# Kernel optimization log

Hardware: AMD Instinct MI355X
Metric: run time of the kernel (lower is better)

The kernel has to match this reference:

```python
import math
import jax, jax.numpy as jnp
import numpy as np

B, T, C = 2, 2048, 4096
H = 32
D = C // H  # head_dim = 128


def compute_freq(dim, max_len, theta=10000):
    freq = 1.0 / theta ** (jnp.arange(0, dim, 2, dtype=jnp.float32) / dim)
    t = jnp.arange(max_len, dtype=jnp.float32)
    m = jnp.einsum('i,j->ij', t, freq)          # [L, dim/2]
    m = jnp.concatenate([m, m], axis=-1)         # [L, dim]
    return jnp.cos(m), jnp.sin(m)


def rotate_half(x):
    # Faithful to source: depth = full last dim, so x1 is the whole tensor
    # and x2 is empty -> rotate_half(x) == x (a quirk of the original code).
    depth = x.shape[-1]
    x1 = x[..., :depth]
    x2 = x[..., depth:]
    return jnp.concatenate([-x2, x1], axis=-1)


def setup_inputs() -> dict:
    key = jax.random.key(0)
    kx, kq, kk, kv, ko = jax.random.split(key, 5)
    std = 0.02
    input_ids = jax.random.normal(kx, (B, T, C), dtype=jnp.float32)
    Wq = jax.random.normal(kq, (C, C), dtype=jnp.float32) * std
    Wk = jax.random.normal(kk, (C, C), dtype=jnp.float32) * std
    Wv = jax.random.normal(kv, (C, C), dtype=jnp.float32) * std
    Wo = jax.random.normal(ko, (C, C), dtype=jnp.float32) * std
    # Additive causal mask, as typically passed to this module.
    causal = jnp.tril(jnp.ones((T, T), dtype=bool))
    attention_mask = jnp.where(causal, 0.0, -1e9).astype(jnp.float32)[None, None]
    return {"input_ids": input_ids, "Wq": Wq, "Wk": Wk, "Wv": Wv,
            "Wo": Wo, "attention_mask": attention_mask}


def reference(input_ids, Wq, Wk, Wv, Wo, attention_mask):
    b, t, c = input_ids.shape
    # QKV projections (no bias), reshape to [b, h, t, d]
    q = (input_ids @ Wq).reshape(b, t, H, D).swapaxes(1, 2)
    k = (input_ids @ Wk).reshape(b, t, H, D).swapaxes(1, 2)
    v = (input_ids @ Wv).reshape(b, t, H, D).swapaxes(1, 2)
    # Inline RoPE (faithful, including the source's rotate_half behavior)
    cos, sin = compute_freq(D, t)                # [t, D]
    q = q * cos + rotate_half(q) * sin
    k = k * cos + rotate_half(k) * sin
    # Naive full attention
    attn = jnp.einsum('bhqd,bhkd->bhqk', q, k) / math.sqrt(D)
    attn = attn + attention_mask
    attn = jax.nn.softmax(attn, axis=-1)
    out = jnp.einsum('bhqk,bhkd->bhqd', attn, v)
    out = out.swapaxes(1, 2).reshape(b, t, c)
    return out @ Wo
```

## Files before the change

### kernel.cpp

```cpp
#include <hip/hip_runtime.h>
#include <hip/hip_bf16.h>

#define B_ 2
#define T_ 2048
#define C_ 4096
#define H_ 32
#define D_ 128

typedef __bf16 bf16x8 __attribute__((ext_vector_type(8)));
typedef float f32x4 __attribute__((ext_vector_type(4)));

__device__ __forceinline__ void gload_lds16(const void* g, void* l) {
  __builtin_amdgcn_global_load_lds(
      (const __attribute__((address_space(1))) void*)g,
      (__attribute__((address_space(3))) void*)l, 16, 0, 0);
}

__device__ __forceinline__ ushort f2bf(float f) {
  union { float f; uint u; } x; x.f = f;
  uint r = x.u + 0x7FFFu + ((x.u >> 16) & 1u);
  return (ushort)(r >> 16);
}

__global__ __launch_bounds__(256) void cvt_f32_bf16(
    const float* __restrict__ in, ushort* __restrict__ out)
{
  long i = ((long)blockIdx.x * 256 + threadIdx.x) * 8;
  float4 a = *(const float4*)&in[i];
  float4 b = *(const float4*)&in[i + 4];
  union { ushort u[8]; uint4 v; } g;
  g.u[0] = f2bf(a.x); g.u[1] = f2bf(a.y); g.u[2] = f2bf(a.z); g.u[3] = f2bf(a.w);
  g.u[4] = f2bf(b.x); g.u[5] = f2bf(b.y); g.u[6] = f2bf(b.z); g.u[7] = f2bf(b.w);
  *(uint4*)&out[i] = g.v;
}

__global__ __launch_bounds__(256) void transpose_f32_bf16(
    const float* __restrict__ in, ushort* __restrict__ out, int ldi, int ldo)
{
  __shared__ __align__(16) ushort tile[64][72];
  const float* ip = in + (long)blockIdx.y * 64 * ldi + (long)blockIdx.x * 64;
  ushort* op = out + (long)blockIdx.x * 64 * ldo + (long)blockIdx.y * 64;
  const int t = threadIdx.x;
  const int row = t >> 2, c0 = (t & 3) * 16;
#pragma unroll
  for (int v = 0; v < 4; ++v) {
    float4 f = *(const float4*)&ip[(long)row * ldi + c0 + v * 4];
    ushort4 w;
    w.x = f2bf(f.x); w.y = f2bf(f.y); w.z = f2bf(f.z); w.w = f2bf(f.w);
    *(ushort4*)&tile[row][c0 + v * 4] = w;
  }
  __syncthreads();
#pragma unroll
  for (int i = 0; i < 2; ++i) {
    int t2 = i * 256 + t;
    int orow = t2 >> 3, ch = t2 & 7;
    union { ushort u[8]; uint4 v; } g;
#pragma unroll
    for (int e = 0; e < 8; ++e) g.u[e] = tile[ch * 8 + e][orow];
    *(uint4*)&op[(long)orow * ldo + ch * 8] = g.v;
  }
}

__global__ __launch_bounds__(256) void transpose_bf16(
    const ushort* __restrict__ in, ushort* __restrict__ out,
    int ldi, int ldo, long zi1, long zi2, long zo1, long zo2)
{
  __shared__ __align__(16) ushort tile[64][72];
  const int z = blockIdx.z;
  const long z1 = z & 31, z2 = z >> 5;
  const ushort* ip = in + z1 * zi1 + z2 * zi2 +
                     (long)blockIdx.y * 64 * ldi + (long)blockIdx.x * 64;
  ushort* op = out + z1 * zo1 + z2 * zo2 +
               (long)blockIdx.x * 64 * ldo + (long)blockIdx.y * 64;
  const int t = threadIdx.x;
#pragma unroll
  for (int i = 0; i < 2; ++i) {
    int t2 = i * 256 + t;
    int row = t2 >> 3, ch = t2 & 7;
    *(uint4*)&tile[row][ch * 8] = *(const uint4*)&ip[(long)row * ldi + ch * 8];
  }
  __syncthreads();
#pragma unroll
  for (int i = 0; i < 2; ++i) {
    int t2 = i * 256 + t;
    int orow = t2 >> 3, ch = t2 & 7;
    union { ushort u[8]; uint4 v; } g;
#pragma unroll
    for (int e = 0; e < 8; ++e) g.u[e] = tile[ch * 8 + e][orow];
    *(uint4*)&op[(long)orow * ldo + ch * 8] = g.v;
  }
}

#define STAGE_A(h, tt) do {                                                    \
    __hip_bfloat16* dst_ = AS + ((((tt) & 1) * 2 + (h)) * 8192) + w * 512;     \
    const __hip_bfloat16* src_ = Asrc + (size_t)((h) * 128) * K + (size_t)(tt) * 64; \
    gload_lds16(src_, dst_);                                                   \
    gload_lds16(src_ + (size_t)64 * K, dst_ + 4096);                           \
  } while (0)

#define STAGE_B(h, tt) do {                                                    \
    __hip_bfloat16* dst_ = BS + ((((tt) & 1) * 2 + (h)) * 8192) + w * 512;     \
    const __hip_bfloat16* src_ = Bsrc + (size_t)((h) * 128) * K + (size_t)(tt) * 64; \
    gload_lds16(src_, dst_);                                                   \
    gload_lds16(src_ + (size_t)64 * K, dst_ + 4096);                           \
  } while (0)

#define MFMA16(pM, pN, AF, BF)                                                 \
  _Pragma("unroll")                                                            \
  for (int mf = 0; mf < 4; ++mf)                                               \
    _Pragma("unroll")                                                          \
    for (int nf = 0; nf < 2; ++nf)                                             \
      _Pragma("unroll")                                                        \
      for (int ks = 0; ks < 2; ++ks)                                           \
        acc[pM][pN][mf][nf] = __builtin_amdgcn_mfma_f32_16x16x32_bf16(         \
            AF[mf][ks], BF[nf][ks], acc[pM][pN][mf][nf], 0, 0, 0);

template <typename OutT>
__global__ __launch_bounds__(512, 2) void gemm256(
    const __hip_bfloat16* __restrict__ A,
    const __hip_bfloat16* __restrict__ Bt,
    OutT* __restrict__ C,
    int M, int N, int K, int rope_mode)
{
  extern __shared__ __hip_bfloat16 smem[];
  __hip_bfloat16* AS = smem;
  __hip_bfloat16* BS = smem + 32768;

  const int tid = threadIdx.x, lane = tid & 63, w = tid >> 6;
  const int wm = w >> 2, wn = w & 3;
  const int fr = lane & 15, quad = lane >> 4;

  const int bid = blockIdx.x;
  const int s = (bid & 7) * 32 + (bid >> 3);
  const int m0 = (s >> 4) * 256, n0 = (s & 15) * 256;

  const int srow = tid >> 3;
  const int schunk = ((tid & 7) ^ (srow & 7)) * 8;
  const __hip_bfloat16* Asrc = A + (size_t)(m0 + srow) * K + schunk;
  const __hip_bfloat16* Bsrc = Bt + (size_t)(n0 + srow) * K + schunk;

  f32x4 acc[2][2][4][2] = {};

  STAGE_A(0, 0); STAGE_B(0, 0); STAGE_A(1, 0); STAGE_B(1, 0);
  STAGE_A(0, 1); STAGE_B(0, 1); STAGE_A(1, 1); STAGE_B(1, 1);
  asm volatile("s_waitcnt vmcnt(8)" ::: "memory");
  asm volatile("s_barrier" ::: "memory");

  const int NT = K >> 6;
  for (int t = 0; t < NT; ++t) {
    const __hip_bfloat16* As0 = AS + (t & 1) * 16384;
    const __hip_bfloat16* Bs0 = BS + (t & 1) * 16384;
    bf16x8 af[4][2], b0[2][2], b1[2][2];

#pragma unroll
    for (int mf = 0; mf < 4; ++mf) {
      const int row = wm * 64 + mf * 16 + fr;
#pragma unroll
      for (int ks = 0; ks < 2; ++ks)
        af[mf][ks] = *(const bf16x8*)
            &As0[row * 64 + (((ks * 4 + quad) ^ (fr & 7)) << 3)];
    }
#pragma unroll
    for (int nf = 0; nf < 2; ++nf) {
      const int row = wn * 32 + nf * 16 + fr;
#pragma unroll
      for (int ks = 0; ks < 2; ++ks)
        b0[nf][ks] = *(const bf16x8*)
            &Bs0[row * 64 + (((ks * 4 + quad) ^ (fr & 7)) << 3)];
    }
    asm volatile("s_barrier" ::: "memory");
    asm volatile("s_waitcnt lgkmcnt(0)" ::: "memory");
    __builtin_amdgcn_s_setprio(1);
    MFMA16(0, 0, af, b0)
    __builtin_amdgcn_s_setprio(0);
    asm volatile("s_barrier" ::: "memory");

#pragma unroll
    for (int nf = 0; nf < 2; ++nf) {
      const int row = wn * 32 + nf * 16 + fr;
#pragma unroll
      for (int ks = 0; ks < 2; ++ks)
        b1[nf][ks] = *(const bf16x8*)
            &Bs0[8192 + row * 64 + (((ks * 4 + quad) ^ (fr & 7)) << 3)];
    }
    if (t + 2 < NT) { STAGE_B(0, t + 2); STAGE_A(0, t + 2); }
    asm volatile("s_barrier" ::: "memory");
    asm volatile("s_waitcnt lgkmcnt(0)" ::: "memory");
    __builtin_amdgcn_s_setprio(1);
    MFMA16(0, 1, af, b1)
    __builtin_amdgcn_s_setprio(0);
    asm volatile("s_barrier" ::: "memory");

#pragma unroll
    for (int mf = 0; mf < 4; ++mf) {
      const int row = wm * 64 + mf * 16 + fr;
#pragma unroll
      for (int ks = 0; ks < 2; ++ks)
        af[mf][ks] = *(const bf16x8*)
            &As0[8192 + row * 64 + (((ks * 4 + quad) ^ (fr & 7)) << 3)];
    }
    if (t + 2 < NT) STAGE_B(1, t + 2);
    asm volatile("s_barrier" ::: "memory");
    asm volatile("s_waitcnt lgkmcnt(0)" ::: "memory");
    __builtin_amdgcn_s_setprio(1);
    MFMA16(1, 1, af, b1)
    __builtin_amdgcn_s_setprio(0);
    asm volatile("s_barrier" ::: "memory");

    if (t + 2 < NT) STAGE_A(1, t + 2);
    if (t < NT - 2) asm volatile("s_waitcnt vmcnt(8)" ::: "memory");
    else            asm volatile("s_waitcnt vmcnt(0)" ::: "memory");
    asm volatile("s_barrier" ::: "memory");
    __builtin_amdgcn_s_setprio(1);
    MFMA16(1, 0, af, b0)
    __builtin_amdgcn_s_setprio(0);
    asm volatile("s_barrier" ::: "memory");
  }

  const float gscale = (rope_mode == 1) ? 0.08838834764831845f : 1.0f;
  float freqv[2] = {0.f, 0.f};
  if (rope_mode) {
#pragma unroll
    for (int nf = 0; nf < 2; ++nf)
      freqv[nf] = exp2f((float)((wn & 1) * 32 + nf * 16 + fr) *
                        -0.20762050593046012f);
  }
#pragma unroll
  for (int pM = 0; pM < 2; ++pM)
#pragma unroll
    for (int mf = 0; mf < 4; ++mf)
#pragma unroll
      for (int r = 0; r < 4; ++r) {
        const int grow = m0 + pM * 128 + wm * 64 + mf * 16 + quad * 4 + r;
        float fct[2] = {1.f, 1.f};
        if (rope_mode) {
          const int tt = grow & (T_ - 1);
#pragma unroll
          for (int nf = 0; nf < 2; ++nf) {
            float sn, cs;
            sincosf((float)tt * freqv[nf], &sn, &cs);
            fct[nf] = (cs + sn) * gscale;
          }
        }
#pragma unroll
        for (int pN = 0; pN < 2; ++pN)
#pragma unroll
          for (int nf = 0; nf < 2; ++nf) {
            const int col = n0 + pN * 128 + wn * 32 + nf * 16 + fr;
            float v = acc[pM][pN][mf][nf][r] * fct[nf];
            if constexpr (sizeof(OutT) == 4)
              C[(size_t)grow * N + col] = v;
            else
              C[(size_t)grow * N + col] = __float2bfloat16(v);
          }
      }
}

__global__ __launch_bounds__(256, 2) void flash_attn(
    const __hip_bfloat16* __restrict__ Q,
    const __hip_bfloat16* __restrict__ K,
    const __hip_bfloat16* __restrict__ Vt,
    __hip_bfloat16* __restrict__ O)
{
  __shared__ __align__(16) __hip_bfloat16 Ks[128 * 128];
  __shared__ __align__(16) __hip_bfloat16 Ps[4][32 * 64];
  const int tid = threadIdx.x, lane = tid & 63, wid = tid >> 6;
  const int bx = blockIdx.x, bh = blockIdx.y;
  const int b = bh >> 5, h = bh & 31;
  const int fr = lane & 15;
  const int quad = lane >> 4;
  const __hip_bfloat16* Kbase = K + (size_t)(b * T_) * C_ + h * D_;
  const __hip_bfloat16* Vbase = Vt + (size_t)bh * D_ * T_;

  const int strow = wid * 32 + quad;

  for (int pass = 0; pass < 2; ++pass) {
    const int qt = pass ? (15 - bx) : bx;
    const int q0 = qt * 128;
    const __hip_bfloat16* Qbase = Q + (size_t)(b * T_ + q0) * C_ + h * D_;

#pragma unroll
    for (int j = 0; j < 8; ++j) {
      const int swz = quad + (j & 1) * 4;
      gload_lds16(Qbase + (size_t)(strow + j * 4) * C_ + ((fr ^ swz) * 8),
                  &Ks[(wid * 8 + j) * 512]);
    }
    __syncthreads();
    bf16x8 qf[2][4];
#pragma unroll
    for (int mi = 0; mi < 2; ++mi)
#pragma unroll
      for (int ks = 0; ks < 4; ++ks)
        qf[mi][ks] = *(const bf16x8*)&Ks[(wid * 32 + mi * 16 + fr) * 128 +
                                         (((ks * 4 + quad) ^ (fr & 7)) << 3)];
    __syncthreads();

    float m_i[2][4], l_i[2][4];
#pragma unroll
    for (int mi = 0; mi < 2; ++mi)
#pragma unroll
      for (int r = 0; r < 4; ++r) { m_i[mi][r] = -1e30f; l_i[mi][r] = 0.f; }
    f32x4 oa[2][8] = {};

    for (int kt = 0; kt <= qt; ++kt) {
#pragma unroll
      for (int j = 0; j < 8; ++j) {
        const int swz = quad + (j & 1) * 4;
        gload_lds16(
            Kbase + (size_t)(kt * 128 + strow + j * 4) * C_ + ((fr ^ swz) * 8),
            &Ks[(wid * 8 + j) * 512]);
      }
      __syncthreads();

      f32x4 s[2][8] = {};
#pragma unroll
      for (int ks = 0; ks < 4; ++ks) {
        bf16x8 kf[8];
#pragma unroll
        for (int ni = 0; ni < 8; ++ni)
          kf[ni] = *(const bf16x8*)&Ks[(ni * 16 + fr) * 128 +
                                       (((ks * 4 + quad) ^ (fr & 7)) << 3)];
        __builtin_amdgcn_s_setprio(1);
#pragma unroll
        for (int mi = 0; mi < 2; ++mi)
#pragma unroll
          for (int ni = 0; ni < 8; ++ni)
            s[mi][ni] = __builtin_amdgcn_mfma_f32_16x16x32_bf16(
                qf[mi][ks], kf[ni], s[mi][ni], 0, 0, 0);
        __builtin_amdgcn_s_setprio(0);
      }
      __syncthreads();

#pragma unroll
      for (int j = 0; j < 8; ++j) {
        const int swz = quad + (j & 1) * 4;
        gload_lds16(
            Vbase + (size_t)(strow + j * 4) * T_ + kt * 128 + ((fr ^ swz) * 8),
            &Ks[(wid * 8 + j) * 512]);
      }

      if (kt == qt) {
#pragma unroll
        for (int mi = 0; mi < 2; ++mi)
#pragma unroll
          for (int ni = 0; ni < 8; ++ni)
#pragma unroll
            for (int r = 0; r < 4; ++r) {
              int rl = wid * 32 + mi * 16 + quad * 4 + r;
              int cl = ni * 16 + fr;
              if (cl > rl) s[mi][ni][r] = -1e30f;
            }
      }

#pragma unroll
      for (int mi = 0; mi < 2; ++mi)
#pragma unroll
        for (int r = 0; r < 4; ++r) {
          float mx = -1e30f;
#pragma unroll
          for (int ni = 0; ni < 8; ++ni) mx = fmaxf(mx, s[mi][ni][r]);
          mx = fmaxf(mx, __shfl_xor(mx, 1, 16));
          mx = fmaxf(mx, __shfl_xor(mx, 2, 16));
          mx = fmaxf(mx, __shfl_xor(mx, 4, 16));
          mx = fmaxf(mx, __shfl_xor(mx, 8, 16));
          float mnew = fmaxf(m_i[mi][r], mx);
          float alpha = __expf(m_i[mi][r] - mnew);
          float rs = 0.f;
#pragma unroll
          for (int ni = 0; ni < 8; ++ni) {
            float p = __expf(s[mi][ni][r] - mnew);
            s[mi][ni][r] = p;
            rs += p;
          }
          rs += __shfl_xor(rs, 1, 16);
          rs += __shfl_xor(rs, 2, 16);
          rs += __shfl_xor(rs, 4, 16);
          rs += __shfl_xor(rs, 8, 16);
          m_i[mi][r] = mnew;
          l_i[mi][r] = l_i[mi][r] * alpha + rs;
#pragma unroll
          for (int ni = 0; ni < 8; ++ni) oa[mi][ni][r] *= alpha;
        }

#pragma unroll
      for (int hh = 0; hh < 2; ++hh) {
#pragma unroll
        for (int mi = 0; mi < 2; ++mi)
#pragma unroll
          for (int l = 0; l < 4; ++l) {
            const int sw = (l ^ quad) & 3;
#pragma unroll
            for (int r = 0; r < 4; ++r)
              Ps[wid][(mi * 16 + quad * 4 + r) * 64 + sw * 16 + fr] =
                  __float2bfloat16(s[mi][hh * 4 + l][r]);
          }
        if (hh == 0) __syncthreads();
#pragma unroll
        for (int kl = 0; kl < 2; ++kl) {
          const int ks = hh * 2 + kl;
          bf16x8 pf[2], vf[8];
#pragma unroll
          for (int mi = 0; mi < 2; ++mi) {
            const int rowl = mi * 16 + fr;
            const int sw = ((kl * 2 + (quad >> 1)) ^ ((fr >> 2) & 3)) & 3;
            pf[mi] = *(const bf16x8*)
                &Ps[wid][rowl * 64 + sw * 16 + (quad & 1) * 8];
          }
#pragma unroll
          for (int ni = 0; ni < 8; ++ni)
            vf[ni] = *(const bf16x8*)&Ks[(ni * 16 + fr) * 128 +
                                         (((ks * 4 + quad) ^ (fr & 7)) << 3)];
          __builtin_amdgcn_s_setprio(1);
#pragma unroll
          for (int mi = 0; mi < 2; ++mi)
#pragma unroll
            for (int ni = 0; ni < 8; ++ni)
              oa[mi][ni] = __builtin_amdgcn_mfma_f32_16x16x32_bf16(
                  pf[mi], vf[ni], oa[mi][ni], 0, 0, 0);
          __builtin_amdgcn_s_setprio(0);
        }
      }
      __syncthreads();
    }

#pragma unroll
    for (int mi = 0; mi < 2; ++mi)
#pragma unroll
      for (int r = 0; r < 4; ++r) {
        float inv = 1.f / l_i[mi][r];
        int grow = b * T_ + q0 + wid * 32 + mi * 16 + quad * 4 + r;
#pragma unroll
        for (int ni = 0; ni < 8; ++ni)
          O[(size_t)grow * C_ + h * D_ + ni * 16 + fr] =
              __float2bfloat16(oa[mi][ni][r] * inv);
      }
  }
}

extern "C" void kernel_launch(void* const* d_in, const int* in_sizes, int n_in,
                              void* d_out, int out_size, void* d_ws, size_t ws_size,
                              hipStream_t stream) {
  const float* X  = (const float*)d_in[0];
  const float* Wq = (const float*)d_in[1];
  const float* Wk = (const float*)d_in[2];
  const float* Wv = (const float*)d_in[3];
  const float* Wo = (const float*)d_in[4];
  float* out = (float*)d_out;

  char* ws = (char*)d_ws;
  const size_t SZ = (size_t)4096 * 4096 * 2;
  __hip_bfloat16* Xb  = (__hip_bfloat16*)(ws);
  __hip_bfloat16* Wt  = (__hip_bfloat16*)(ws + SZ);
  __hip_bfloat16* Qb  = (__hip_bfloat16*)(ws + 2 * SZ);
  __hip_bfloat16* Kb  = (__hip_bfloat16*)(ws + 3 * SZ);
  __hip_bfloat16* Vb  = (__hip_bfloat16*)(ws + 4 * SZ);
  __hip_bfloat16* Vtb = Xb;
  __hip_bfloat16* Ob  = Vb;

  const dim3 blk(256);
  const dim3 gT(64, 64, 1);

  hipFuncSetAttribute(reinterpret_cast<const void*>(&gemm256<__hip_bfloat16>),
                      hipFuncAttributeMaxDynamicSharedMemorySize, 131072);
  hipFuncSetAttribute(reinterpret_cast<const void*>(&gemm256<float>),
                      hipFuncAttributeMaxDynamicSharedMemorySize, 131072);

  cvt_f32_bf16<<<8192, blk, 0, stream>>>(X, (ushort*)Xb);

  transpose_f32_bf16<<<gT, blk, 0, stream>>>(Wq, (ushort*)Wt, 4096, 4096);
  gemm256<__hip_bfloat16><<<dim3(256), dim3(512), 131072, stream>>>(
      Xb, Wt, Qb, 4096, 4096, 4096, 1);
  transpose_f32_bf16<<<gT, blk, 0, stream>>>(Wk, (ushort*)Wt, 4096, 4096);
  gemm256<__hip_bfloat16><<<dim3(256), dim3(512), 131072, stream>>>(
      Xb, Wt, Kb, 4096, 4096, 4096, 2);
  transpose_f32_bf16<<<gT, blk, 0, stream>>>(Wv, (ushort*)Wt, 4096, 4096);
  gemm256<__hip_bfloat16><<<dim3(256), dim3(512), 131072, stream>>>(
      Xb, Wt, Vb, 4096, 4096, 4096, 0);

  transpose_bf16<<<dim3(2, 32, 64), blk, 0, stream>>>(
      (const ushort*)Vb, (ushort*)Vtb, 4096, 2048,
       128,  8388608,  262144,  8388608);

  flash_attn<<<dim3(8, 64), blk, 0, stream>>>(Qb, Kb, Vtb, Ob);

  transpose_f32_bf16<<<gT, blk, 0, stream>>>(Wo, (ushort*)Wt, 4096, 4096);
  gemm256<float><<<dim3(256), dim3(512), 131072, stream>>>(
      Ob, Wt, out, 4096, 4096, 4096, 0);
}
```

Measured before the change: 1.014 ms.

## Fuse Q/K/V projections into one 768-block GEMM with 32-wide K tiles

Result: slower. 1.093 ms (+7.7%).

```diff
diff --git a/kernel.cpp b/kernel.cpp
--- a/kernel.cpp
+++ b/kernel.cpp
@@ -91,14 +91,14 @@
   }
 }
 
-#define STAGE_A(h, tt) do {                                                    \
+#define STAGE_A64(h, tt) do {                                                  \
     __hip_bfloat16* dst_ = AS + ((((tt) & 1) * 2 + (h)) * 8192) + w * 512;     \
     const __hip_bfloat16* src_ = Asrc + (size_t)((h) * 128) * K + (size_t)(tt) * 64; \
     gload_lds16(src_, dst_);                                                   \
     gload_lds16(src_ + (size_t)64 * K, dst_ + 4096);                           \
   } while (0)
 
-#define STAGE_B(h, tt) do {                                                    \
+#define STAGE_B64(h, tt) do {                                                  \
     __hip_bfloat16* dst_ = BS + ((((tt) & 1) * 2 + (h)) * 8192) + w * 512;     \
     const __hip_bfloat16* src_ = Bsrc + (size_t)((h) * 128) * K + (size_t)(tt) * 64; \
     gload_lds16(src_, dst_);                                                   \
@@ -141,8 +141,8 @@
 
   f32x4 acc[2][2][4][2] = {};
 
-  STAGE_A(0, 0); STAGE_B(0, 0); STAGE_A(1, 0); STAGE_B(1, 0);
-  STAGE_A(0, 1); STAGE_B(0, 1); STAGE_A(1, 1); STAGE_B(1, 1);
+  STAGE_A64(0, 0); STAGE_B64(0, 0); STAGE_A64(1, 0); STAGE_B64(1, 0);
+  STAGE_A64(0, 1); STAGE_B64(0, 1); STAGE_A64(1, 1); STAGE_B64(1, 1);
   asm volatile("s_waitcnt vmcnt(8)" ::: "memory");
   asm volatile("s_barrier" ::: "memory");
 
@@ -183,7 +183,7 @@
         b1[nf][ks] = *(const bf16x8*)
             &Bs0[8192 + row * 64 + (((ks * 4 + quad) ^ (fr & 7)) << 3)];
     }
-    if (t + 2 < NT) { STAGE_B(0, t + 2); STAGE_A(0, t + 2); }
+    if (t + 2 < NT) { STAGE_B64(0, t + 2); STAGE_A64(0, t + 2); }
     asm volatile("s_barrier" ::: "memory");
     asm volatile("s_waitcnt lgkmcnt(0)" ::: "memory");
     __builtin_amdgcn_s_setprio(1);
@@ -199,7 +199,7 @@
         af[mf][ks] = *(const bf16x8*)
             &As0[8192 + row * 64 + (((ks * 4 + quad) ^ (fr & 7)) << 3)];
     }
-    if (t + 2 < NT) STAGE_B(1, t + 2);
+    if (t + 2 < NT) STAGE_B64(1, t + 2);
     asm volatile("s_barrier" ::: "memory");
     asm volatile("s_waitcnt lgkmcnt(0)" ::: "memory");
     __builtin_amdgcn_s_setprio(1);
@@ -207,7 +207,7 @@
     __builtin_amdgcn_s_setprio(0);
     asm volatile("s_barrier" ::: "memory");
 
-    if (t + 2 < NT) STAGE_A(1, t + 2);
+    if (t + 2 < NT) STAGE_A64(1, t + 2);
     if (t < NT - 2) asm volatile("s_waitcnt vmcnt(8)" ::: "memory");
     else            asm volatile("s_waitcnt vmcnt(0)" ::: "memory");
     asm volatile("s_barrier" ::: "memory");
@@ -252,6 +252,159 @@
               C[(size_t)grow * N + col] = v;
             else
               C[(size_t)grow * N + col] = __float2bfloat16(v);
+          }
+      }
+}
+
+#define STAGE_A32(h, tt) do {                                                  \
+    __hip_bfloat16* dst_ = AS + ((((tt) & 1) * 2 + (h)) * 4096) + w * 512;     \
+    gload_lds16(Asrc + (size_t)((h) * 128) * K + (size_t)(tt) * 32, dst_);     \
+  } while (0)
+
+#define STAGE_B32(h, tt) do {                                                  \
+    __hip_bfloat16* dst_ = BS + ((((tt) & 1) * 2 + (h)) * 4096) + w * 512;     \
+    gload_lds16(Bsrc + (size_t)((h) * 128) * K + (size_t)(tt) * 32, dst_);     \
+  } while (0)
+
+#define MFMA8(pM, pN, AF, BF)                                                  \
+  _Pragma("unroll")                                                            \
+  for (int mf = 0; mf < 4; ++mf)                                               \
+    _Pragma("unroll")                                                          \
+    for (int nf = 0; nf < 2; ++nf)                                             \
+      acc[pM][pN][mf][nf] = __builtin_amdgcn_mfma_f32_16x16x32_bf16(           \
+          AF[mf], BF[nf], acc[pM][pN][mf][nf], 0, 0, 0);
+
+__global__ __launch_bounds__(512, 2) void gemm256_qkv(
+    const __hip_bfloat16* __restrict__ A,
+    const __hip_bfloat16* __restrict__ Bq,
+    const __hip_bfloat16* __restrict__ Bk,
+    const __hip_bfloat16* __restrict__ Bv,
+    __hip_bfloat16* __restrict__ Cq,
+    __hip_bfloat16* __restrict__ Ck,
+    __hip_bfloat16* __restrict__ Cv,
+    int N, int K)
+{
+  extern __shared__ __hip_bfloat16 smem[];
+  __hip_bfloat16* AS = smem;
+  __hip_bfloat16* BS = smem + 16384;
+
+  const int tid = threadIdx.x, lane = tid & 63, w = tid >> 6;
+  const int wm = w >> 2, wn = w & 3;
+  const int fr = lane & 15, quad = lane >> 4;
+
+  const int bid = blockIdx.x;
+  const int s = (bid & 7) * 96 + (bid >> 3);
+  const int mi = s / 48, ni = s % 48;
+  const int m0 = mi * 256;
+  const int wsel = ni >> 4;
+  const int n0 = (ni & 15) * 256;
+  const __hip_bfloat16* Bt = wsel == 0 ? Bq : (wsel == 1 ? Bk : Bv);
+  __hip_bfloat16* C = wsel == 0 ? Cq : (wsel == 1 ? Ck : Cv);
+  const int rope_mode = wsel == 0 ? 1 : (wsel == 1 ? 2 : 0);
+
+  const int srow = tid >> 2;
+  const int schunk = ((tid & 3) ^ (srow & 3)) * 8;
+  const __hip_bfloat16* Asrc = A + (size_t)(m0 + srow) * K + schunk;
+  const __hip_bfloat16* Bsrc = Bt + (size_t)(n0 + srow) * K + schunk;
+
+  f32x4 acc[2][2][4][2] = {};
+
+  STAGE_A32(0, 0); STAGE_B32(0, 0); STAGE_A32(1, 0); STAGE_B32(1, 0);
+  STAGE_A32(0, 1); STAGE_B32(0, 1); STAGE_A32(1, 1); STAGE_B32(1, 1);
+  asm volatile("s_waitcnt vmcnt(4)" ::: "memory");
+  asm volatile("s_barrier" ::: "memory");
+
+  const int NT = K >> 5;
+  for (int t = 0; t < NT; ++t) {
+    const __hip_bfloat16* As0 = AS + (t & 1) * 8192;
+    const __hip_bfloat16* Bs0 = BS + (t & 1) * 8192;
+    bf16x8 af[4], b0[2], b1[2];
+
+#pragma unroll
+    for (int mf = 0; mf < 4; ++mf) {
+      const int row = wm * 64 + mf * 16 + fr;
+      af[mf] = *(const bf16x8*)&As0[row * 32 + ((quad ^ (fr & 3)) << 3)];
+    }
+#pragma unroll
+    for (int nf = 0; nf < 2; ++nf) {
+      const int row = wn * 32 + nf * 16 + fr;
+      b0[nf] = *(const bf16x8*)&Bs0[row * 32 + ((quad ^ (fr & 3)) << 3)];
+    }
+    asm volatile("s_barrier" ::: "memory");
+    asm volatile("s_waitcnt lgkmcnt(0)" ::: "memory");
+    __builtin_amdgcn_s_setprio(1);
+    MFMA8(0, 0, af, b0)
+    __builtin_amdgcn_s_setprio(0);
+    asm volatile("s_barrier" ::: "memory");
+
+#pragma unroll
+    for (int nf = 0; nf < 2; ++nf) {
+      const int row = wn * 32 + nf * 16 + fr;
+      b1[nf] = *(const bf16x8*)&Bs0[4096 + row * 32 + ((quad ^ (fr & 3)) << 3)];
+    }
+    if (t + 2 < NT) { STAGE_B32(0, t + 2); STAGE_A32(0, t + 2); }
+    asm volatile("s_barrier" ::: "memory");
+    asm volatile("s_waitcnt lgkmcnt(0)" ::: "memory");
+    __builtin_amdgcn_s_setprio(1);
+    MFMA8(0, 1, af, b1)
+    __builtin_amdgcn_s_setprio(0);
+    asm volatile("s_barrier" ::: "memory");
+
+#pragma unroll
+    for (int mf = 0; mf < 4; ++mf) {
+      const int row = wm * 64 + mf * 16 + fr;
+      af[mf] = *(const bf16x8*)&As0[4096 + row * 32 + ((quad ^ (fr & 3)) << 3)];
+    }
+    if (t + 2 < NT) STAGE_B32(1, t + 2);
+    asm volatile("s_barrier" ::: "memory");
+    asm volatile("s_waitcnt lgkmcnt(0)" ::: "memory");
+    __builtin_amdgcn_s_setprio(1);
+    MFMA8(1, 1, af, b1)
+    __builtin_amdgcn_s_setprio(0);
+    asm volatile("s_barrier" ::: "memory");
+
+    if (t + 2 < NT) STAGE_A32(1, t + 2);
+    if (t < NT - 2) asm volatile("s_waitcnt vmcnt(4)" ::: "memory");
+    else            asm volatile("s_waitcnt vmcnt(0)" ::: "memory");
+    asm volatile("s_barrier" ::: "memory");
+    __builtin_amdgcn_s_setprio(1);
+    MFMA8(1, 0, af, b0)
+    __builtin_amdgcn_s_setprio(0);
+    asm volatile("s_barrier" ::: "memory");
+  }
+
+  const float gscale = (rope_mode == 1) ? 0.08838834764831845f : 1.0f;
+  float freqv[2] = {0.f, 0.f};
+  if (rope_mode) {
+#pragma unroll
+    for (int nf = 0; nf < 2; ++nf)
+      freqv[nf] = exp2f((float)((wn & 1) * 32 + nf * 16 + fr) *
+                        -0.20762050593046012f);
+  }
+#pragma unroll
+  for (int pM = 0; pM < 2; ++pM)
+#pragma unroll
+    for (int mf = 0; mf < 4; ++mf)
+#pragma unroll
+      for (int r = 0; r < 4; ++r) {
+        const int grow = m0 + pM * 128 + wm * 64 + mf * 16 + quad * 4 + r;
+        float fct[2] = {1.f, 1.f};
+        if (rope_mode) {
+          const int tt = grow & (T_ - 1);
+#pragma unroll
+          for (int nf = 0; nf < 2; ++nf) {
+            float sn, cs;
+            sincosf((float)tt * freqv[nf], &sn, &cs);
+            fct[nf] = (cs + sn) * gscale;
+          }
+        }
+#pragma unroll
+        for (int pN = 0; pN < 2; ++pN)
+#pragma unroll
+          for (int nf = 0; nf < 2; ++nf) {
+            const int col = n0 + pN * 128 + wn * 32 + nf * 16 + fr;
+            C[(size_t)grow * N + col] =
+                __float2bfloat16(acc[pM][pN][mf][nf][r] * fct[nf]);
           }
       }
 }
@@ -449,14 +602,6 @@
 
   char* ws = (char*)d_ws;
   const size_t SZ = (size_t)4096 * 4096 * 2;
-  __hip_bfloat16* Xb  = (__hip_bfloat16*)(ws);
-  __hip_bfloat16* Wt  = (__hip_bfloat16*)(ws + SZ);
-  __hip_bfloat16* Qb  = (__hip_bfloat16*)(ws + 2 * SZ);
-  __hip_bfloat16* Kb  = (__hip_bfloat16*)(ws + 3 * SZ);
-  __hip_bfloat16* Vb  = (__hip_bfloat16*)(ws + 4 * SZ);
-  __hip_bfloat16* Vtb = Xb;
-  __hip_bfloat16* Ob  = Vb;
-
   const dim3 blk(256);
   const dim3 gT(64, 64, 1);
 
@@ -464,26 +609,63 @@
                       hipFuncAttributeMaxDynamicSharedMemorySize, 131072);
   hipFuncSetAttribute(reinterpret_cast<const void*>(&gemm256<float>),
                       hipFuncAttributeMaxDynamicSharedMemorySize, 131072);
-
-  cvt_f32_bf16<<<8192, blk, 0, stream>>>(X, (ushort*)Xb);
-
-  transpose_f32_bf16<<<gT, blk, 0, stream>>>(Wq, (ushort*)Wt, 4096, 4096);
-  gemm256<__hip_bfloat16><<<dim3(256), dim3(512), 131072, stream>>>(
-      Xb, Wt, Qb, 4096, 4096, 4096, 1);
-  transpose_f32_bf16<<<gT, blk, 0, stream>>>(Wk, (ushort*)Wt, 4096, 4096);
-  gemm256<__hip_bfloat16><<<dim3(256), dim3(512), 131072, stream>>>(
-      Xb, Wt, Kb, 4096, 4096, 4096, 2);
-  transpose_f32_bf16<<<gT, blk, 0, stream>>>(Wv, (ushort*)Wt, 4096, 4096);
-  gemm256<__hip_bfloat16><<<dim3(256), dim3(512), 131072, stream>>>(
-      Xb, Wt, Vb, 4096, 4096, 4096, 0);
-
-  transpose_bf16<<<dim3(2, 32, 64), blk, 0, stream>>>(
-      (const ushort*)Vb, (ushort*)Vtb, 4096, 2048,
-       128,  8388608,  262144,  8388608);
-
-  flash_attn<<<dim3(8, 64), blk, 0, stream>>>(Qb, Kb, Vtb, Ob);
-
-  transpose_f32_bf16<<<gT, blk, 0, stream>>>(Wo, (ushort*)Wt, 4096, 4096);
-  gemm256<float><<<dim3(256), dim3(512), 131072, stream>>>(
-      Ob, Wt, out, 4096, 4096, 4096, 0);
-}
+  hipFuncSetAttribute(reinterpret_cast<const void*>(&gemm256_qkv),
+                      hipFuncAttributeMaxDynamicSharedMemorySize, 65536);
+
+  if (ws_size >= 7 * SZ) {
+    __hip_bfloat16* Xb  = (__hip_bfloat16*)(ws);
+    __hip_bfloat16* Wqt = (__hip_bfloat16*)(ws + SZ);
+    __hip_bfloat16* Wkt = (__hip_bfloat16*)(ws + 2 * SZ);
+    __hip_bfloat16* Wvt = (__hip_bfloat16*)(ws + 3 * SZ);
+    __hip_bfloat16* Qb  = (__hip_bfloat16*)(ws + 4 * SZ);
+    __hip_bfloat16* Kb  = (__hip_bfloat16*)(ws + 5 * SZ);
+    __hip_bfloat16* Vb  = (__hip_bfloat16*)(ws + 6 * SZ);
+    __hip_bfloat16* Vtb = Xb;
+    __hip_bfloat16* Ob  = Vb;
+    __hip_bfloat16* Wt  = Wkt;
+
+    cvt_f32_bf16<<<8192, blk, 0, stream>>>(X, (ushort*)Xb);
+    transpose_f32_bf16<<<gT, blk, 0, stream>>>(Wq, (ushort*)Wqt, 4096, 4096);
+    transpose_f32_bf16<<<gT, blk, 0, stream>>>(Wk, (ushort*)Wkt, 4096, 4096);
+    transpose_f32_bf16<<<gT, blk, 0, stream>>>(Wv, (ushort*)Wvt, 4096, 4096);
+
+    gemm256_qkv<<<dim3(768), dim3(512), 65536, stream>>>(
+        Xb, Wqt, Wkt, Wvt, Qb, Kb, Vb, 4096, 4096);
+
+    transpose_bf16<<<dim3(2, 32, 64), blk, 0, stream>>>(
+        (const ushort*)Vb, (ushort*)Vtb, 4096, 2048,
+        128, 8388608, 262144, 8388608);
+
+    flash_attn<<<dim3(8, 64), blk, 0, stream>>>(Qb, Kb, Vtb, Ob);
+
+    transpose_f32_bf16<<<gT, blk, 0, stream>>>(Wo, (ushort*)Wt, 4096, 4096);
+    gemm256<float><<<dim3(256), dim3(512), 131072, stream>>>(
+        Ob, Wt, out, 4096, 4096, 4096, 0);
+  } else {
+    __hip_bfloat16* Xb  = (__hip_bfloat16*)(ws);
+    __hip_bfloat16* Wt  = (__hip_bfloat16*)(ws + SZ);
+    __hip_bfloat16* Qb  = (__hip_bfloat16*)(ws + 2 * SZ);
+    __hip_bfloat16* Kb  = (__hip_bfloat16*)(ws + 3 * SZ);
+    __hip_bfloat16* Vb  = (__hip_bfloat16*)(ws + 4 * SZ);
+    __hip_bfloat16* Vtb = Xb;
+    __hip_bfloat16* Ob  = Vb;
+
+    cvt_f32_bf16<<<8192, blk, 0, stream>>>(X, (ushort*)Xb);
+    transpose_f32_bf16<<<gT, blk, 0, stream>>>(Wq, (ushort*)Wt, 4096, 4096);
+    gemm256<__hip_bfloat16><<<dim3(256), dim3(512), 131072, stream>>>(
+        Xb, Wt, Qb, 4096, 4096, 4096, 1);
+    transpose_f32_bf16<<<gT, blk, 0, stream>>>(Wk, (ushort*)Wt, 4096, 4096);
+    gemm256<__hip_bfloat16><<<dim3(256), dim3(512), 131072, stream>>>(
+        Xb, Wt, Kb, 4096, 4096, 4096, 2);
+    transpose_f32_bf16<<<gT, blk, 0, stream>>>(Wv, (ushort*)Wt, 4096, 4096);
+    gemm256<__hip_bfloat16><<<dim3(256), dim3(512), 131072, stream>>>(
+        Xb, Wt, Vb, 4096, 4096, 4096, 0);
+    transpose_bf16<<<dim3(2, 32, 64), blk, 0, stream>>>(
+        (const ushort*)Vb, (ushort*)Vtb, 4096, 2048,
+        128, 8388608, 262144, 8388608);
+    flash_attn<<<dim3(8, 64), blk, 0, stream>>>(Qb, Kb, Vtb, Ob);
+    transpose_f32_bf16<<<gT, blk, 0, stream>>>(Wo, (ushort*)Wt, 4096, 4096);
+    gemm256<float><<<dim3(256), dim3(512), 131072, stream>>>(
+        Ob, Wt, out, 4096, 4096, 4096, 0);
+  }
+}
```

## Fuse Q, K, V projections into one 768-block GEMM launch

Applied to the files above, without the earlier changes.

Measured after the change: 1.024 ms. About the same (+1.0%).

```diff
diff --git a/kernel.cpp b/kernel.cpp
--- a/kernel.cpp
+++ b/kernel.cpp
@@ -91,14 +91,14 @@
   }
 }
 
-#define STAGE_A(h, tt) do {                                                    \
+#define STAGE_A64(h, tt) do {                                                  \
     __hip_bfloat16* dst_ = AS + ((((tt) & 1) * 2 + (h)) * 8192) + w * 512;     \
     const __hip_bfloat16* src_ = Asrc + (size_t)((h) * 128) * K + (size_t)(tt) * 64; \
     gload_lds16(src_, dst_);                                                   \
     gload_lds16(src_ + (size_t)64 * K, dst_ + 4096);                           \
   } while (0)
 
-#define STAGE_B(h, tt) do {                                                    \
+#define STAGE_B64(h, tt) do {                                                  \
     __hip_bfloat16* dst_ = BS + ((((tt) & 1) * 2 + (h)) * 8192) + w * 512;     \
     const __hip_bfloat16* src_ = Bsrc + (size_t)((h) * 128) * K + (size_t)(tt) * 64; \
     gload_lds16(src_, dst_);                                                   \
@@ -114,6 +114,118 @@
       for (int ks = 0; ks < 2; ++ks)                                           \
         acc[pM][pN][mf][nf] = __builtin_amdgcn_mfma_f32_16x16x32_bf16(         \
             AF[mf][ks], BF[nf][ks], acc[pM][pN][mf][nf], 0, 0, 0);
+
+#define GEMM_KLOOP()                                                           \
+  STAGE_A64(0, 0); STAGE_B64(0, 0); STAGE_A64(1, 0); STAGE_B64(1, 0);          \
+  STAGE_A64(0, 1); STAGE_B64(0, 1); STAGE_A64(1, 1); STAGE_B64(1, 1);          \
+  asm volatile("s_waitcnt vmcnt(8)" ::: "memory");                             \
+  asm volatile("s_barrier" ::: "memory");                                      \
+  const int NT = K >> 6;                                                       \
+  for (int t = 0; t < NT; ++t) {                                               \
+    const __hip_bfloat16* As0 = AS + (t & 1) * 16384;                          \
+    const __hip_bfloat16* Bs0 = BS + (t & 1) * 16384;                          \
+    bf16x8 af[4][2], b0[2][2], b1[2][2];                                       \
+    _Pragma("unroll")                                                          \
+    for (int mf = 0; mf < 4; ++mf) {                                           \
+      const int row = wm * 64 + mf * 16 + fr;                                  \
+      _Pragma("unroll")                                                        \
+      for (int ks = 0; ks < 2; ++ks)                                           \
+        af[mf][ks] = *(const bf16x8*)                                          \
+            &As0[row * 64 + (((ks * 4 + quad) ^ (fr & 7)) << 3)];              \
+    }                                                                          \
+    _Pragma("unroll")                                                          \
+    for (int nf = 0; nf < 2; ++nf) {                                           \
+      const int row = wn * 32 + nf * 16 + fr;                                  \
+      _Pragma("unroll")                                                        \
+      for (int ks = 0; ks < 2; ++ks)                                           \
+        b0[nf][ks] = *(const bf16x8*)                                          \
+            &Bs0[row * 64 + (((ks * 4 + quad) ^ (fr & 7)) << 3)];              \
+    }                                                                          \
+    asm volatile("s_barrier" ::: "memory");                                    \
+    asm volatile("s_waitcnt lgkmcnt(0)" ::: "memory");                         \
+    __builtin_amdgcn_s_setprio(1);                                             \
+    MFMA16(0, 0, af, b0)                                                       \
+    __builtin_amdgcn_s_setprio(0);                                             \
+    asm volatile("s_barrier" ::: "memory");                                    \
+    _Pragma("unroll")                                                          \
+    for (int nf = 0; nf < 2; ++nf) {                                           \
+      const int row = wn * 32 + nf * 16 + fr;                                  \
+      _Pragma("unroll")                                                        \
+      for (int ks = 0; ks < 2; ++ks)                                           \
+        b1[nf][ks] = *(const bf16x8*)                                          \
+            &Bs0[8192 + row * 64 + (((ks * 4 + quad) ^ (fr & 7)) << 3)];       \
+    }                                                                          \
+    if (t + 2 < NT) { STAGE_B64(0, t + 2); STAGE_A64(0, t + 2); }              \
+    asm volatile("s_barrier" ::: "memory");                                    \
+    asm volatile("s_waitcnt lgkmcnt(0)" ::: "memory");                         \
+    __builtin_amdgcn_s_setprio(1);                                             \
+    MFMA16(0, 1, af, b1)                                                       \
+    __builtin_amdgcn_s_setprio(0);                                             \
+    asm volatile("s_barrier" ::: "memory");                                    \
+    _Pragma("unroll")                                                          \
+    for (int mf = 0; mf < 4; ++mf) {                                           \
+      const int row = wm * 64 + mf * 16 + fr;                                  \
+      _Pragma("unroll")                                                        \
+      for (int ks = 0; ks < 2; ++ks)                                           \
+        af[mf][ks] = *(const bf16x8*)                                          \
+            &As0[8192 + row * 64 + (((ks * 4 + quad) ^ (fr & 7)) << 3)];       \
+    }                                                                          \
+    if (t + 2 < NT) STAGE_B64(1, t + 2);                                       \
+    asm volatile("s_barrier" ::: "memory");                                    \
+    asm volatile("s_waitcnt lgkmcnt(0)" ::: "memory");                         \
+    __builtin_amdgcn_s_setprio(1);                                             \
+    MFMA16(1, 1, af, b1)                                                       \
+    __builtin_amdgcn_s_setprio(0);                                             \
+    asm volatile("s_barrier" ::: "memory");                                    \
+    if (t + 2 < NT) STAGE_A64(1, t + 2);                                       \
+    if (t < NT - 2) asm volatile("s_waitcnt vmcnt(8)" ::: "memory");           \
+    else            asm volatile("s_waitcnt vmcnt(0)" ::: "memory");           \
+    asm volatile("s_barrier" ::: "memory");                                    \
+    __builtin_amdgcn_s_setprio(1);                                             \
+    MFMA16(1, 0, af, b0)                                                       \
+    __builtin_amdgcn_s_setprio(0);                                             \
+    asm volatile("s_barrier" ::: "memory");                                    \
+  }
+
+#define GEMM_EPILOGUE(CPTR, NCOLS, BF16OUT)                                    \
+  const float gscale = (rope_mode == 1) ? 0.08838834764831845f : 1.0f;         \
+  float freqv[2] = {0.f, 0.f};                                                 \
+  if (rope_mode) {                                                             \
+    _Pragma("unroll")                                                          \
+    for (int nf = 0; nf < 2; ++nf)                                             \
+      freqv[nf] = exp2f((float)((wn & 1) * 32 + nf * 16 + fr) *                \
+                        -0.20762050593046012f);                                \
+  }                                                                            \
+  _Pragma("unroll")                                                            \
+  for (int pM = 0; pM < 2; ++pM)                                               \
+    _Pragma("unroll")                                                          \
+    for (int mf = 0; mf < 4; ++mf)                                             \
+      _Pragma("unroll")                                                        \
+      for (int r = 0; r < 4; ++r) {                                            \
+        const int grow = m0 + pM * 128 + wm * 64 + mf * 16 + quad * 4 + r;     \
+        float fct[2] = {1.f, 1.f};                                             \
+        if (rope_mode) {                                                       \
+          const int tt = grow & (T_ - 1);                                      \
+          _Pragma("unroll")                                                    \
+          for (int nf = 0; nf < 2; ++nf) {                                     \
+            float sn, cs;                                                      \
+            sincosf((float)tt * freqv[nf], &sn, &cs);                          \
+            fct[nf] = (cs + sn) * gscale;                                      \
+          }                                                                    \
+        }                                                                      \
+        _Pragma("unroll")                                                      \
+        for (int pN = 0; pN < 2; ++pN)                                         \
+          _Pragma("unroll")                                                    \
+          for (int nf = 0; nf < 2; ++nf) {                                     \
+            const int col = n0 + pN * 128 + wn * 32 + nf * 16 + fr;            \
+            float v = acc[pM][pN][mf][nf][r] * fct[nf];                        \
+            if (BF16OUT)                                                       \
+              ((__hip_bfloat16*)(CPTR))[(size_t)grow * (NCOLS) + col] =        \
+                  __float2bfloat16(v);                                         \
+            else                                                               \
+              ((float*)(CPTR))[(size_t)grow * (NCOLS) + col] = v;              \
+          }                                                                    \
+      }
 
 template <typename OutT>
 __global__ __launch_bounds__(512, 2) void gemm256(
@@ -140,120 +252,47 @@
   const __hip_bfloat16* Bsrc = Bt + (size_t)(n0 + srow) * K + schunk;
 
   f32x4 acc[2][2][4][2] = {};
-
-  STAGE_A(0, 0); STAGE_B(0, 0); STAGE_A(1, 0); STAGE_B(1, 0);
-  STAGE_A(0, 1); STAGE_B(0, 1); STAGE_A(1, 1); STAGE_B(1, 1);
-  asm volatile("s_waitcnt vmcnt(8)" ::: "memory");
-  asm volatile("s_barrier" ::: "memory");
-
-  const int NT = K >> 6;
-  for (int t = 0; t < NT; ++t) {
-    const __hip_bfloat16* As0 = AS + (t & 1) * 16384;
-    const __hip_bfloat16* Bs0 = BS + (t & 1) * 16384;
-    bf16x8 af[4][2], b0[2][2], b1[2][2];
-
-#pragma unroll
-    for (int mf = 0; mf < 4; ++mf) {
-      const int row = wm * 64 + mf * 16 + fr;
-#pragma unroll
-      for (int ks = 0; ks < 2; ++ks)
-        af[mf][ks] = *(const bf16x8*)
-            &As0[row * 64 + (((ks * 4 + quad) ^ (fr & 7)) << 3)];
-    }
-#pragma unroll
-    for (int nf = 0; nf < 2; ++nf) {
-      const int row = wn * 32 + nf * 16 + fr;
-#pragma unroll
-      for (int ks = 0; ks < 2; ++ks)
-        b0[nf][ks] = *(const bf16x8*)
-            &Bs0[row * 64 + (((ks * 4 + quad) ^ (fr & 7)) << 3)];
-    }
-    asm volatile("s_barrier" ::: "memory");
-    asm volatile("s_waitcnt lgkmcnt(0)" ::: "memory");
-    __builtin_amdgcn_s_setprio(1);
-    MFMA16(0, 0, af, b0)
-    __builtin_amdgcn_s_setprio(0);
-    asm volatile("s_barrier" ::: "memory");
-
-#pragma unroll
-    for (int nf = 0; nf < 2; ++nf) {
-      const int row = wn * 32 + nf * 16 + fr;
-#pragma unroll
-      for (int ks = 0; ks < 2; ++ks)
-        b1[nf][ks] = *(const bf16x8*)
-            &Bs0[8192 + row * 64 + (((ks * 4 + quad) ^ (fr & 7)) << 3)];
-    }
-    if (t + 2 < NT) { STAGE_B(0, t + 2); STAGE_A(0, t + 2); }
-    asm volatile("s_barrier" ::: "memory");
-    asm volatile("s_waitcnt lgkmcnt(0)" ::: "memory");
-    __builtin_amdgcn_s_setprio(1);
-    MFMA16(0, 1, af, b1)
-    __builtin_amdgcn_s_setprio(0);
-    asm volatile("s_barrier" ::: "memory");
-
-#pragma unroll
-    for (int mf = 0; mf < 4; ++mf) {
-      const int row = wm * 64 + mf * 16 + fr;
-#pragma unroll
-      for (int ks = 0; ks < 2; ++ks)
-        af[mf][ks] = *(const bf16x8*)
-            &As0[8192 + row * 64 + (((ks * 4 + quad) ^ (fr & 7)) << 3)];
-    }
-    if (t + 2 < NT) STAGE_B(1, t + 2);
-    asm volatile("s_barrier" ::: "memory");
-    asm volatile("s_waitcnt lgkmcnt(0)" ::: "memory");
-    __builtin_amdgcn_s_setprio(1);
-    MFMA16(1, 1, af, b1)
-    __builtin_amdgcn_s_setprio(0);
-    asm volatile("s_barrier" ::: "memory");
-
-    if (t + 2 < NT) STAGE_A(1, t + 2);
-    if (t < NT - 2) asm volatile("s_waitcnt vmcnt(8)" ::: "memory");
-    else            asm volatile("s_waitcnt vmcnt(0)" ::: "memory");
-    asm volatile("s_barrier" ::: "memory");
-    __builtin_amdgcn_s_setprio(1);
-    MFMA16(1, 0, af, b0)
-    __builtin_amdgcn_s_setprio(0);
-    asm volatile("s_barrier" ::: "memory");
-  }
-
-  const float gscale = (rope_mode == 1) ? 0.08838834764831845f : 1.0f;
-  float freqv[2] = {0.f, 0.f};
-  if (rope_mode) {
-#pragma unroll
-    for (int nf = 0; nf < 2; ++nf)
-      freqv[nf] = exp2f((float)((wn & 1) * 32 + nf * 16 + fr) *
-                        -0.20762050593046012f);
-  }
-#pragma unroll
-  for (int pM = 0; pM < 2; ++pM)
-#pragma unroll
-    for (int mf = 0; mf < 4; ++mf)
-#pragma unroll
-      for (int r = 0; r < 4; ++r) {
-        const int grow = m0 + pM * 128 + wm * 64 + mf * 16 + quad * 4 + r;
-        float fct[2] = {1.f, 1.f};
-        if (rope_mode) {
-          const int tt = grow & (T_ - 1);
-#pragma unroll
-          for (int nf = 0; nf < 2; ++nf) {
-            float sn, cs;
-            sincosf((float)tt * freqv[nf], &sn, &cs);
-            fct[nf] = (cs + sn) * gscale;
-          }
-        }
-#pragma unroll
-        for (int pN = 0; pN < 2; ++pN)
-#pragma unroll
-          for (int nf = 0; nf < 2; ++nf) {
-            const int col = n0 + pN * 128 + wn * 32 + nf * 16 + fr;
-            float v = acc[pM][pN][mf][nf][r] * fct[nf];
-            if constexpr (sizeof(OutT) == 4)
-              C[(size_t)grow * N + col] = v;
-            else
-              C[(size_t)grow * N + col] = __float2bfloat16(v);
-          }
-      }
+  GEMM_KLOOP()
+  GEMM_EPILOGUE(C, N, (sizeof(OutT) == 2))
+}
+
+__global__ __launch_bounds__(512, 2) void gemm256_qkv(
+    const __hip_bfloat16* __restrict__ A,
+    const __hip_bfloat16* __restrict__ Bq,
+    const __hip_bfloat16* __restrict__ Bk,
+    const __hip_bfloat16* __restrict__ Bv,
+    __hip_bfloat16* __restrict__ Cq,
+    __hip_bfloat16* __restrict__ Ck,
+    __hip_bfloat16* __restrict__ Cv,
+    int N, int K)
+{
+  extern __shared__ __hip_bfloat16 smem[];
+  __hip_bfloat16* AS = smem;
+  __hip_bfloat16* BS = smem + 32768;
+
+  const int tid = threadIdx.x, lane = tid & 63, w = tid >> 6;
+  const int wm = w >> 2, wn = w & 3;
+  const int fr = lane & 15, quad = lane >> 4;
+
+  const int bid = blockIdx.x;
+  const int xcd = bid & 7, j = bid >> 3;
+  const int ni = xcd * 6 + (j >> 4);
+  const int mi = j & 15;
+  const int m0 = mi * 256;
+  const int wsel = ni >> 4;
+  const int n0 = (ni & 15) * 256;
+  const __hip_bfloat16* Bt = wsel == 0 ? Bq : (wsel == 1 ? Bk : Bv);
+  __hip_bfloat16* C = wsel == 0 ? Cq : (wsel == 1 ? Ck : Cv);
+  const int rope_mode = wsel == 0 ? 1 : (wsel == 1 ? 2 : 0);
+
+  const int srow = tid >> 3;
+  const int schunk = ((tid & 7) ^ (srow & 7)) * 8;
+  const __hip_bfloat16* Asrc = A + (size_t)(m0 + srow) * K + schunk;
+  const __hip_bfloat16* Bsrc = Bt + (size_t)(n0 + srow) * K + schunk;
+
+  f32x4 acc[2][2][4][2] = {};
+  GEMM_KLOOP()
+  GEMM_EPILOGUE(C, N, true)
 }
 
 __global__ __launch_bounds__(256, 2) void flash_attn(
@@ -449,14 +488,6 @@
 
   char* ws = (char*)d_ws;
   const size_t SZ = (size_t)4096 * 4096 * 2;
-  __hip_bfloat16* Xb  = (__hip_bfloat16*)(ws);
-  __hip_bfloat16* Wt  = (__hip_bfloat16*)(ws + SZ);
-  __hip_bfloat16* Qb  = (__hip_bfloat16*)(ws + 2 * SZ);
-  __hip_bfloat16* Kb  = (__hip_bfloat16*)(ws + 3 * SZ);
-  __hip_bfloat16* Vb  = (__hip_bfloat16*)(ws + 4 * SZ);
-  __hip_bfloat16* Vtb = Xb;
-  __hip_bfloat16* Ob  = Vb;
-
   const dim3 blk(256);
   const dim3 gT(64, 64, 1);
 
@@ -464,26 +495,63 @@
                       hipFuncAttributeMaxDynamicSharedMemorySize, 131072);
   hipFuncSetAttribute(reinterpret_cast<const void*>(&gemm256<float>),
                       hipFuncAttributeMaxDynamicSharedMemorySize, 131072);
-
-  cvt_f32_bf16<<<8192, blk, 0, stream>>>(X, (ushort*)Xb);
-
-  transpose_f32_bf16<<<gT, blk, 0, stream>>>(Wq, (ushort*)Wt, 4096, 4096);
-  gemm256<__hip_bfloat16><<<dim3(256), dim3(512), 131072, stream>>>(
-      Xb, Wt, Qb, 4096, 4096, 4096, 1);
-  transpose_f32_bf16<<<gT, blk, 0, stream>>>(Wk, (ushort*)Wt, 4096, 4096);
-  gemm256<__hip_bfloat16><<<dim3(256), dim3(512), 131072, stream>>>(
-      Xb, Wt, Kb, 4096, 4096, 4096, 2);
-  transpose_f32_bf16<<<gT, blk, 0, stream>>>(Wv, (ushort*)Wt, 4096, 4096);
-  gemm256<__hip_bfloat16><<<dim3(256), dim3(512), 131072, stream>>>(
-      Xb, Wt, Vb, 4096, 4096, 4096, 0);
-
-  transpose_bf16<<<dim3(2, 32, 64), blk, 0, stream>>>(
-      (const ushort*)Vb, (ushort*)Vtb, 4096, 2048,
-       128,  8388608,  262144,  8388608);
-
-  flash_attn<<<dim3(8, 64), blk, 0, stream>>>(Qb, Kb, Vtb, Ob);
-
-  transpose_f32_bf16<<<gT, blk, 0, stream>>>(Wo, (ushort*)Wt, 4096, 4096);
-  gemm256<float><<<dim3(256), dim3(512), 131072, stream>>>(
-      Ob, Wt, out, 4096, 4096, 4096, 0);
-}
+  hipFuncSetAttribute(reinterpret_cast<const void*>(&gemm256_qkv),
+                      hipFuncAttributeMaxDynamicSharedMemorySize, 131072);
+
+  if (ws_size >= 7 * SZ) {
+    __hip_bfloat16* Xb  = (__hip_bfloat16*)(ws);
+    __hip_bfloat16* Wqt = (__hip_bfloat16*)(ws + SZ);
+    __hip_bfloat16* Wkt = (__hip_bfloat16*)(ws + 2 * SZ);
+    __hip_bfloat16* Wvt = (__hip_bfloat16*)(ws + 3 * SZ);
+    __hip_bfloat16* Qb  = (__hip_bfloat16*)(ws + 4 * SZ);
+    __hip_bfloat16* Kb  = (__hip_bfloat16*)(ws + 5 * SZ);
+    __hip_bfloat16* Vb  = (__hip_bfloat16*)(ws + 6 * SZ);
+    __hip_bfloat16* Vtb = Xb;
+    __hip_bfloat16* Ob  = Vb;
+    __hip_bfloat16* Wt  = Wkt;
+
+    cvt_f32_bf16<<<8192, blk, 0, stream>>>(X, (ushort*)Xb);
+    transpose_f32_bf16<<<gT, blk, 0, stream>>>(Wq, (ushort*)Wqt, 4096, 4096);
+    transpose_f32_bf16<<<gT, blk, 0, stream>>>(Wk, (ushort*)Wkt, 4096, 4096);
+    transpose_f32_bf16<<<gT, blk, 0, stream>>>(Wv, (ushort*)Wvt, 4096, 4096);
+
+    gemm256_qkv<<<dim3(768), dim3(512), 131072, stream>>>(
+        Xb, Wqt, Wkt, Wvt, Qb, Kb, Vb, 4096, 4096);
+
+    transpose_bf16<<<dim3(2, 32, 64), blk, 0, stream>>>(
+        (const ushort*)Vb, (ushort*)Vtb, 4096, 2048,
+        128, 8388608, 262144, 8388608);
+
+    flash_attn<<<dim3(8, 64), blk, 0, stream>>>(Qb, Kb, Vtb, Ob);
+
+    transpose_f32_bf16<<<gT, blk, 0, stream>>>(Wo, (ushort*)Wt, 4096, 4096);
+    gemm256<float><<<dim3(256), dim3(512), 131072, stream>>>(
+        Ob, Wt, out, 4096, 4096, 4096, 0);
+  } else {
+    __hip_bfloat16* Xb  = (__hip_bfloat16*)(ws);
+    __hip_bfloat16* Wt  = (__hip_bfloat16*)(ws + SZ);
+    __hip_bfloat16* Qb  = (__hip_bfloat16*)(ws + 2 * SZ);
+    __hip_bfloat16* Kb  = (__hip_bfloat16*)(ws + 3 * SZ);
+    __hip_bfloat16* Vb  = (__hip_bfloat16*)(ws + 4 * SZ);
+    __hip_bfloat16* Vtb = Xb;
+    __hip_bfloat16* Ob  = Vb;
+
+    cvt_f32_bf16<<<8192, blk, 0, stream>>>(X, (ushort*)Xb);
+    transpose_f32_bf16<<<gT, blk, 0, stream>>>(Wq, (ushort*)Wt, 4096, 4096);
+    gemm256<__hip_bfloat16><<<dim3(256), dim3(512), 131072, stream>>>(
+        Xb, Wt, Qb, 4096, 4096, 4096, 1);
+    transpose_f32_bf16<<<gT, blk, 0, stream>>>(Wk, (ushort*)Wt, 4096, 4096);
+    gemm256<__hip_bfloat16><<<dim3(256), dim3(512), 131072, stream>>>(
+        Xb, Wt, Kb, 4096, 4096, 4096, 2);
+    transpose_f32_bf16<<<gT, blk, 0, stream>>>(Wv, (ushort*)Wt, 4096, 4096);
+    gemm256<__hip_bfloat16><<<dim3(256), dim3(512), 131072, stream>>>(
+        Xb, Wt, Vb, 4096, 4096, 4096, 0);
+    transpose_bf16<<<dim3(2, 32, 64), blk, 0, stream>>>(
+        (const ushort*)Vb, (ushort*)Vtb, 4096, 2048,
+        128, 8388608, 262144, 8388608);
+    flash_attn<<<dim3(8, 64), blk, 0, stream>>>(Qb, Kb, Vtb, Ob);
+    transpose_f32_bf16<<<gT, blk, 0, stream>>>(Wo, (ushort*)Wt, 4096, 4096);
+    gemm256<float><<<dim3(256), dim3(512), 131072, stream>>>(
+        Ob, Wt, out, 4096, 4096, 4096, 0);
+  }
+}
```
